# Optimization experiments

Hardware: AMD Instinct MI355X
Metric: run time of the kernel (lower is better)

## Reference

```python
import jax, jax.numpy as jnp
import numpy as np

B, T, D, H, DH, W = 2, 2048, 512, 8, 64, 64  # batch, seq, d_model, heads, d_head, window
BASE = 10000.0


def rope(x):
    # x: [b, t, d]; rotate-half RoPE applied over the full feature dim (as in source: pos_enc on d_model)
    d = x.shape[-1]
    half = d // 2
    inv_freq = BASE ** (-jnp.arange(half, dtype=jnp.float32) / half)          # [half]
    ang = jnp.arange(x.shape[1], dtype=jnp.float32)[:, None] * inv_freq       # [t, half]
    cos, sin = jnp.cos(ang), jnp.sin(ang)
    x1, x2 = x[..., :half], x[..., half:]
    return jnp.concatenate([x1 * cos - x2 * sin, x1 * sin + x2 * cos], axis=-1)


def setup_inputs() -> dict:
    key = jax.random.key(0)
    k0, k1, k2, k3 = jax.random.split(key, 4)
    x = jax.random.normal(k0, (B, T, D), jnp.float32)
    Wq = jax.random.normal(k1, (D, D), jnp.float32) / jnp.sqrt(D)
    Wkv = jax.random.normal(k2, (D, 2 * D), jnp.float32) / jnp.sqrt(D)
    # NOTE: source zero-inits lin; we use random weights so the output/grads are non-trivial
    Wlin = jax.random.normal(k3, (D, D), jnp.float32) / jnp.sqrt(D)
    blin = jnp.zeros((D,), jnp.float32)
    return {"x": x, "Wq": Wq, "Wkv": Wkv, "Wlin": Wlin, "blin": blin}


def reference(x, Wq, Wkv, Wlin, blin):
    b, t, _ = x.shape
    scale = DH ** -0.5
    q = rope(x @ Wq).reshape(b, t, H, DH).transpose(0, 2, 1, 3)               # [b,h,t,d]
    kv = x @ Wkv
    k, v = kv[..., :D], kv[..., D:]
    k = rope(k).reshape(b, t, H, DH).transpose(0, 2, 1, 3)                    # [b,h,t,d]
    v = v.reshape(b, t, H, DH).transpose(0, 2, 1, 3)                          # [b,h,t,d]
    pad = [(0, 0), (0, 0), (W - 1, 0), (0, 0)]
    kp, vp = jnp.pad(k, pad), jnp.pad(v, pad)                                 # [b,h,t+W-1,d]
    idx = jnp.arange(t)[:, None] + jnp.arange(W)[None, :]                     # [t,W] sliding-window gather
    kw, vw = kp[:, :, idx], vp[:, :, idx]                                     # [b,h,t,W,d]
    attn = jax.nn.softmax(jnp.einsum('bhtd,bhtwd->bhtw', q, kw) * scale, axis=-1)
    out = jnp.einsum('bhtw,bhtwd->bhtd', attn, vw)                            # [b,h,t,d]
    out = out.transpose(0, 2, 1, 3).reshape(b, t, D)
    return out @ Wlin + blin
```

## Files before the change

### kernel.cpp

```cpp
#include <hip/hip_runtime.h>
#include <cstddef>

#define T_N 2048
#define M_N 4096
#define KW  512

typedef __attribute__((ext_vector_type(4))) float f32x4;
typedef _Float16 f16x8 __attribute__((ext_vector_type(8)));
typedef _Float16 f16x2 __attribute__((ext_vector_type(2)));

#define GLOAD_LDS(g, l) __builtin_amdgcn_global_load_lds( \
    (const __attribute__((address_space(1))) unsigned int*)(g), \
    (__attribute__((address_space(3))) unsigned int*)(l), 16, 0, 0)

__global__ __launch_bounds__(256) void prep(
    const float* __restrict__ x, const float* __restrict__ Wq,
    const float* __restrict__ Wkv, const float* __restrict__ Wlin,
    _Float16* __restrict__ Axp, _Float16* __restrict__ Wcatp,
    _Float16* __restrict__ Wlinp, _Float16* __restrict__ tab16) {
  __shared__ float tile[64][65];
  const int bid = blockIdx.x;
  const int tid = threadIdx.x;
  if (bid < 1024) {
    int idx = bid * 256 + tid;
    int m = idx >> 6, k8 = (idx & 63) << 3;
    const float* src = x + (size_t)m * 512 + k8;
    const float4 a = *(const float4*)src;
    const float4 b = *(const float4*)(src + 4);
    f16x8 o;
    o[0] = (_Float16)a.x; o[1] = (_Float16)a.y; o[2] = (_Float16)a.z; o[3] = (_Float16)a.w;
    o[4] = (_Float16)b.x; o[5] = (_Float16)b.y; o[6] = (_Float16)b.z; o[7] = (_Float16)b.w;
    *(f16x8*)(Axp + (size_t)m * 512 + k8) = o;
    return;
  }
  if (bid >= 1280) {
    int gid = (bid - 1280) * 256 + tid;
    int t = gid >> 8, f = gid & 255;
    float invf = exp2f(-0.05190512648261503f * (float)f);
    float s, c;
    sincosf((float)t * invf, &s, &c);
    f16x2 cs;
    cs[0] = (_Float16)c; cs[1] = (_Float16)s;
    *(f16x2*)(tab16 + 2 * ((size_t)t * 256 + f)) = cs;
    return;
  }
  int wb = bid - 1024;
  const float* W; int N; int mode; int bx, by;
  if (wb < 64)       { W = Wq;   N = 512;  mode = 0; bx = wb & 7;  by = wb >> 3; }
  else if (wb < 192) { wb -= 64;  W = Wkv; N = 1024; mode = 1; bx = wb & 15; by = wb >> 4; }
  else               { wb -= 192; W = Wlin; N = 512; mode = 2; bx = wb & 7;  by = wb >> 3; }
  const int n0 = bx * 64, k0 = by * 64;
#pragma unroll
  for (int it = 0; it < 16; ++it) {
    int idx = tid + it * 256;
    int r = idx >> 6, c = idx & 63;
    tile[r][c] = W[(size_t)(k0 + r) * N + n0 + c];
  }
  __syncthreads();
#pragma unroll
  for (int it = 0; it < 16; ++it) {
    int idx = tid + it * 256;
    int n = idx >> 6, kk = idx & 63;
    int cg = n0 + n;
    int np; _Float16* out;
    if (mode == 0)      { np = 2 * (cg & 255) + (cg >> 8); out = Wcatp; }
    else if (mode == 1) { np = (cg < 512) ? 512 + 2 * (cg & 255) + (cg >> 8)
                                          : 1024 + (cg - 512);
                          out = Wcatp; }
    else                { np = cg; out = Wlinp; }
    out[(size_t)np * KW + k0 + kk] = (_Float16)tile[kk][n];
  }
}

__global__ __launch_bounds__(256) void gemm_qkv_rope(
    const _Float16* __restrict__ Ap, const _Float16* __restrict__ Bp,
    const _Float16* __restrict__ tab16, _Float16* __restrict__ Qh,
    _Float16* __restrict__ Kh, _Float16* __restrict__ Vh) {
  __shared__ __align__(16) _Float16 sm[64 * 64 + 128 * 64];
  _Float16* sA = sm;
  _Float16* sB = sm + 64 * 64;
  const int tid = threadIdx.x;
  const int wid = tid >> 6, lane = tid & 63;
  const int il = lane & 15, g = lane >> 4;
  const int m0 = blockIdx.y * 64, n0 = blockIdx.x * 128;
  const int wm = (wid >> 1) * 32, wn = (wid & 1) * 64;
  f32x4 acc[2][4] = {};

  const _Float16* ga = Ap + (size_t)(m0 + wid * 16 + (lane >> 3)) * KW + (lane & 7) * 8;
  const _Float16* gb = Bp + (size_t)(n0 + wid * 32 + (lane >> 3)) * KW + (lane & 7) * 8;
  _Float16* la = sA + wid * 16 * 64;
  _Float16* lb = sB + wid * 32 * 64;

  for (int k0 = 0; k0 < KW; k0 += 64) {
    GLOAD_LDS(ga + k0, la);
    GLOAD_LDS(ga + 8 * KW + k0, la + 8 * 64);
#pragma unroll
    for (int p = 0; p < 4; ++p)
      GLOAD_LDS(gb + (size_t)(p * 8) * KW + k0, lb + p * 8 * 64);
    __syncthreads();
#pragma unroll
    for (int ks = 0; ks < 2; ++ks) {
      f16x8 af[2], bf[4];
#pragma unroll
      for (int i = 0; i < 2; ++i)
        af[i] = *(const f16x8*)&sA[(wm + i * 16 + il) * 64 + ks * 32 + g * 8];
#pragma unroll
      for (int j = 0; j < 4; ++j)
        bf[j] = *(const f16x8*)&sB[(wn + j * 16 + il) * 64 + ks * 32 + g * 8];
#pragma unroll
      for (int i = 0; i < 2; ++i)
#pragma unroll
        for (int j = 0; j < 4; ++j)
          acc[i][j] = __builtin_amdgcn_mfma_f32_16x16x32_f16(af[i], bf[j], acc[i][j], 0, 0, 0);
    }
    __syncthreads();
  }
  const int b8 = (m0 >> 11) * 8;
  const int tb = m0 & (T_N - 1);
  const bool isv = (n0 >= 1024);
  const bool isk = (n0 >= 512) && !isv;
  _Float16* OT  = sm;
  _Float16* OTV = sm;

  if (isv) {
#pragma unroll
    for (int i = 0; i < 2; ++i)
#pragma unroll
      for (int j = 0; j < 4; ++j) {
        f32x4 v = acc[i][j];
        int col = wn + 16 * j + il;
#pragma unroll
        for (int r = 0; r < 4; ++r) {
          int tl = wm + i * 16 + g * 4 + r;
          OTV[col * 72 + tl] = (_Float16)v[r];
        }
      }
    __syncthreads();
    const int cv = n0 - 1024;
#pragma unroll
    for (int it = 0; it < 4; ++it) {
      int c = tid + it * 256;
      int col = c >> 3, t8 = (c & 7) * 8;
      int h = (cv + col) >> 6, d = (cv + col) & 63;
      *(f16x8*)(Vh + ((size_t)(b8 + h) * 64 + d) * T_N + tb + t8) =
          *(const f16x8*)&OTV[col * 72 + t8];
    }
    return;
  }
  const int n0p = n0 - (isk ? 512 : 0);
  const int h0 = n0p >> 7;
#pragma unroll
  for (int i = 0; i < 2; ++i) {
#pragma unroll
    for (int j = 0; j < 4; ++j) {
      f32x4 v = acc[i][j];
#pragma unroll
      for (int r = 0; r < 4; ++r) {
        float self = v[r];
        float part = __shfl_xor(self, 1);
        int tl = wm + i * 16 + g * 4 + r;
        int tpos = tb + tl;
        int p = il & 1;
        int f = (n0p + wn + 16 * j + (il & 14)) >> 1;
        f16x2 cs = *(const f16x2*)(tab16 + 2 * ((size_t)tpos * 256 + f));
        float c = (float)cs[0], s = (float)cs[1];
        float o = p ? (self * c + part * s) : (self * c - part * s);
        OT[(p * 64 + tl) * 72 + (f & 63)] = (_Float16)o;
      }
    }
  }
  __syncthreads();
  _Float16* dst = isk ? Kh : Qh;
#pragma unroll
  for (int it = 0; it < 4; ++it) {
    int c = tid + it * 256;
    int p = c >> 9, row = (c >> 3) & 63, d8 = (c & 7) * 8;
    *(f16x8*)(dst + ((size_t)(b8 + h0 + 4 * p) * T_N + tb + row) * 64 + d8) =
        *(const f16x8*)&OT[(p * 64 + row) * 72 + d8];
  }
}

#define RQ 72
#define RK 72
#define RV 104
#define RP 104
#define RO 72

__global__ __launch_bounds__(256, 4) void attn_fused(
    const _Float16* __restrict__ Qh, const _Float16* __restrict__ Kh,
    const _Float16* __restrict__ Vh, _Float16* __restrict__ Aout) {
  __shared__ __align__(16) _Float16 sm[19200];
  __shared__ float pm[2][32];
  __shared__ float ps[2][32];
  _Float16* Ks  = sm;
  _Float16* Qs  = sm + 6912;
  _Float16* VTs = sm + 9216;
  _Float16* Ps  = sm + 15872;
  _Float16* OH  = sm;

  const int wgid = blockIdx.x;
  const int orig = (wgid & 7) * 128 + (wgid >> 3);
  const int tile = orig & 63;
  const int h = (orig >> 6) & 7;
  const int b = orig >> 9;
  const int t0 = tile * 32;
  const int tid = threadIdx.x;
  const size_t bh = (size_t)(b * 8 + h);

  {
    int i = tid >> 3, d8 = (tid & 7) * 8;
    *(f16x8*)(Qs + i * RQ + d8) =
        *(const f16x8*)(Qh + (bh * T_N + t0 + i) * 64 + d8);
  }
#pragma unroll
  for (int itn = 0; itn < 3; ++itn) {
    int c = tid + itn * 256;
    int jr = c >> 3, d8 = (c & 7) * 8;
    int p = t0 - 64 + jr;
    f16x8 o = {};
    if (p >= 0) o = *(const f16x8*)(Kh + (bh * T_N + p) * 64 + d8);
    *(f16x8*)(Ks + jr * RK + d8) = o;
  }
#pragma unroll
  for (int itn = 0; itn < 3; ++itn) {
    int c = tid + itn * 256;
    int d = c & 63, jr8 = (c >> 6) * 8;
    int p8 = t0 - 64 + jr8;
    f16x8 o = {};
    if (p8 >= 0) o = *(const f16x8*)(Vh + (bh * 64 + d) * T_N + p8);
    *(f16x8*)(VTs + d * RV + jr8) = o;
  }
  __syncthreads();

  const int lane = tid & 63;
  const int il = lane & 15, g = lane >> 4;
  const int w = tid >> 6;
  const int it = w & 1, jh = w >> 1;
  const int i_q = 16 * it + il;

  f32x4 sacc[3] = {};
  {
    f16x8 qf0 = *(const f16x8*)(Qs + i_q * RQ + 8 * g);
    f16x8 qf1 = *(const f16x8*)(Qs + i_q * RQ + 32 + 8 * g);
#pragma unroll
    for (int jt = 0; jt < 3; ++jt) {
      int jrow = 16 * (3 * jh + jt) + il;
      f16x8 a0 = *(const f16x8*)(Ks + jrow * RK + 8 * g);
      f16x8 a1 = *(const f16x8*)(Ks + jrow * RK + 32 + 8 * g);
      sacc[jt] = __builtin_amdgcn_mfma_f32_16x16x32_f16(a0, qf0, sacc[jt], 0, 0, 0);
      sacc[jt] = __builtin_amdgcn_mfma_f32_16x16x32_f16(a1, qf1, sacc[jt], 0, 0, 0);
    }
  }
  float mx = -3e38f;
#pragma unroll
  for (int jt = 0; jt < 3; ++jt)
#pragma unroll
    for (int r = 0; r < 4; ++r) {
      int j = 16 * (3 * jh + jt) + 4 * g + r;
      int wv = j - 1 - i_q;
      if (wv >= 0 && wv < 64) mx = fmaxf(mx, sacc[jt][r]);
    }
  mx = fmaxf(mx, __shfl_xor(mx, 16));
  mx = fmaxf(mx, __shfl_xor(mx, 32));
  if (g == 0) pm[jh][i_q] = mx;
  __syncthreads();
  {
    const float m = fmaxf(pm[0][i_q], pm[1][i_q]);
    float sum = 0.f;
#pragma unroll
    for (int jt = 0; jt < 3; ++jt)
#pragma unroll
      for (int r = 0; r < 4; ++r) {
        int j = 16 * (3 * jh + jt) + 4 * g + r;
        int wv = j - 1 - i_q;
        float ex = 0.f;
        if (wv >= 0 && wv < 64) {
          ex = exp2f((sacc[jt][r] - m) * 0.18033688011112042f);
          sum += ex;
        }
        Ps[i_q * RP + j] = (_Float16)ex;
      }
    sum += __shfl_xor(sum, 16);
    sum += __shfl_xor(sum, 32);
    if (g == 0) ps[jh][i_q] = sum;
  }
  __syncthreads();

  f32x4 oacc[2] = {};
#pragma unroll
  for (int ks = 0; ks < 3; ++ks) {
    f16x8 pf = *(const f16x8*)(Ps + i_q * RP + 32 * ks + 8 * g);
#pragma unroll
    for (int q2 = 0; q2 < 2; ++q2) {
      int dt = jh + 2 * q2;
      f16x8 vf = *(const f16x8*)(VTs + (16 * dt + il) * RV + 32 * ks + 8 * g);
      oacc[q2] = __builtin_amdgcn_mfma_f32_16x16x32_f16(pf, vf, oacc[q2], 0, 0, 0);
    }
  }
#pragma unroll
  for (int r = 0; r < 4; ++r) {
    int i = 16 * it + 4 * g + r;
    float inv = 1.f / (ps[0][i] + ps[1][i]);
#pragma unroll
    for (int q2 = 0; q2 < 2; ++q2) {
      int d = 16 * (jh + 2 * q2) + il;
      OH[i * RO + d] = (_Float16)(oacc[q2][r] * inv);
    }
  }
  __syncthreads();
  {
    int i = tid >> 3, d8 = (tid & 7) * 8;
    *(f16x8*)(Aout + ((size_t)(b * T_N + t0 + i)) * 512 + h * 64 + d8) =
        *(const f16x8*)(OH + i * RO + d8);
  }
}

__global__ __launch_bounds__(256) void gemm_out(
    const _Float16* __restrict__ Ap, const _Float16* __restrict__ Bp,
    const float* __restrict__ bias, float* __restrict__ C) {
  __shared__ __align__(16) _Float16 sA[64 * 64];
  __shared__ __align__(16) _Float16 sB[64 * 64];
  const int tid = threadIdx.x;
  const int wid = tid >> 6, lane = tid & 63;
  const int il = lane & 15, g = lane >> 4;
  const int m0 = blockIdx.y * 64, n0 = blockIdx.x * 64;
  const int wm = (wid >> 1) * 32, wn = (wid & 1) * 32;
  f32x4 acc[2][2] = {};

  const _Float16* ga = Ap + (size_t)(m0 + wid * 16 + (lane >> 3)) * KW + (lane & 7) * 8;
  const _Float16* gb = Bp + (size_t)(n0 + wid * 16 + (lane >> 3)) * KW + (lane & 7) * 8;
  _Float16* la = sA + wid * 16 * 64;
  _Float16* lb = sB + wid * 16 * 64;

  for (int k0 = 0; k0 < KW; k0 += 64) {
    GLOAD_LDS(ga + k0, la);
    GLOAD_LDS(ga + 8 * KW + k0, la + 8 * 64);
    GLOAD_LDS(gb + k0, lb);
    GLOAD_LDS(gb + 8 * KW + k0, lb + 8 * 64);
    __syncthreads();
#pragma unroll
    for (int ks = 0; ks < 2; ++ks) {
      f16x8 af[2], bf[2];
#pragma unroll
      for (int i = 0; i < 2; ++i)
        af[i] = *(const f16x8*)&sA[(wm + i * 16 + il) * 64 + ks * 32 + g * 8];
#pragma unroll
      for (int j = 0; j < 2; ++j)
        bf[j] = *(const f16x8*)&sB[(wn + j * 16 + il) * 64 + ks * 32 + g * 8];
#pragma unroll
      for (int i = 0; i < 2; ++i)
#pragma unroll
        for (int j = 0; j < 2; ++j)
          acc[i][j] = __builtin_amdgcn_mfma_f32_16x16x32_f16(af[i], bf[j], acc[i][j], 0, 0, 0);
    }
    __syncthreads();
  }
  const int cn = n0 + wn + il;
  const int rbase = m0 + wm + g * 4;
#pragma unroll
  for (int j = 0; j < 2; ++j) {
    float badd = bias[cn + j * 16];
#pragma unroll
    for (int i = 0; i < 2; ++i)
#pragma unroll
      for (int r = 0; r < 4; ++r)
        C[(size_t)(rbase + i * 16 + r) * 512 + cn + j * 16] = acc[i][j][r] + badd;
  }
}

extern "C" void kernel_launch(void* const* d_in, const int* in_sizes, int n_in,
                              void* d_out, int out_size, void* d_ws, size_t ws_size,
                              hipStream_t stream) {
  const float* x    = (const float*)d_in[0];
  const float* Wq   = (const float*)d_in[1];
  const float* Wkv  = (const float*)d_in[2];
  const float* Wlin = (const float*)d_in[3];
  const float* blin = (const float*)d_in[4];
  float* out = (float*)d_out;

  char* ws = (char*)d_ws;
  _Float16* Axp   = (_Float16*)(ws);
  _Float16* Wcatp = (_Float16*)(ws + 4194304);
  _Float16* Wlinp = (_Float16*)(ws + 5767168);
  _Float16* tab16 = (_Float16*)(ws + 6291456);
  _Float16* Qh    = (_Float16*)(ws + 8388608);
  _Float16* Kh    = (_Float16*)(ws + 12582912);
  _Float16* Vh    = (_Float16*)(ws + 16777216);
  _Float16* Aaop  = (_Float16*)(ws + 20971520);

  prep<<<3328, 256, 0, stream>>>(x, Wq, Wkv, Wlin, Axp, Wcatp, Wlinp, tab16);
  gemm_qkv_rope<<<dim3(12, 64), 256, 0, stream>>>(Axp, Wcatp, tab16, Qh, Kh, Vh);
  attn_fused<<<1024, 256, 0, stream>>>(Qh, Kh, Vh, Aaop);
  gemm_out<<<dim3(8, 64), 256, 0, stream>>>(Aaop, Wlinp, blin, out);
}
```

Before: 104.1 us.

## Enlarge attention query tile to 64 rows and keep softmax per-wave

The sliding-window attention kernel now processes 64 queries per workgroup instead of 32, so each loaded K/V block (128 keys) is shared by more queries. This cuts redundant K/V loads. Each wave now owns 16 full query rows, so the max and sum reductions stay inside the wave and the cross-wave LDS exchange and two barriers go away. The cost is more LDS per block, launch bounds dropping from 4 to 2 blocks per CU, and half as many workgroups.

```diff
diff --git a/kernel.cpp b/kernel.cpp
--- a/kernel.cpp
+++ b/kernel.cpp
@@ -7,6 +7,7 @@
 
 typedef __attribute__((ext_vector_type(4))) float f32x4;
 typedef _Float16 f16x8 __attribute__((ext_vector_type(8)));
+typedef _Float16 f16x4 __attribute__((ext_vector_type(4)));
 typedef _Float16 f16x2 __attribute__((ext_vector_type(2)));
 
 #define GLOAD_LDS(g, l) __builtin_amdgcn_global_load_lds( \
@@ -180,138 +181,136 @@
   }
 }
 
-#define RQ 72
-#define RK 72
-#define RV 104
-#define RP 104
-#define RO 72
-
-__global__ __launch_bounds__(256, 4) void attn_fused(
+__global__ __launch_bounds__(256, 2) void attn_fused(
     const _Float16* __restrict__ Qh, const _Float16* __restrict__ Kh,
     const _Float16* __restrict__ Vh, _Float16* __restrict__ Aout) {
-  __shared__ __align__(16) _Float16 sm[19200];
-  __shared__ float pm[2][32];
-  __shared__ float ps[2][32];
+  __shared__ __align__(16) _Float16 sm[31232];
   _Float16* Ks  = sm;
-  _Float16* Qs  = sm + 6912;
   _Float16* VTs = sm + 9216;
-  _Float16* Ps  = sm + 15872;
+  _Float16* Qs  = sm + 17920;
+  _Float16* Ps  = sm + 22528;
   _Float16* OH  = sm;
 
   const int wgid = blockIdx.x;
-  const int orig = (wgid & 7) * 128 + (wgid >> 3);
-  const int tile = orig & 63;
-  const int h = (orig >> 6) & 7;
-  const int b = orig >> 9;
-  const int t0 = tile * 32;
+  const int orig = (wgid & 7) * 64 + (wgid >> 3);
+  const int tile = orig & 31;
+  const int h = (orig >> 5) & 7;
+  const int b = orig >> 8;
+  const int t0 = tile * 64;
   const int tid = threadIdx.x;
   const size_t bh = (size_t)(b * 8 + h);
 
-  {
-    int i = tid >> 3, d8 = (tid & 7) * 8;
-    *(f16x8*)(Qs + i * RQ + d8) =
-        *(const f16x8*)(Qh + (bh * T_N + t0 + i) * 64 + d8);
-  }
-#pragma unroll
-  for (int itn = 0; itn < 3; ++itn) {
+#pragma unroll
+  for (int itn = 0; itn < 2; ++itn) {
+    int c = tid + itn * 256;
+    int row = c >> 3, d8 = (c & 7) * 8;
+    *(f16x8*)(Qs + row * 72 + d8) =
+        *(const f16x8*)(Qh + (bh * T_N + t0 + row) * 64 + d8);
+  }
+#pragma unroll
+  for (int itn = 0; itn < 4; ++itn) {
     int c = tid + itn * 256;
     int jr = c >> 3, d8 = (c & 7) * 8;
     int p = t0 - 64 + jr;
     f16x8 o = {};
     if (p >= 0) o = *(const f16x8*)(Kh + (bh * T_N + p) * 64 + d8);
-    *(f16x8*)(Ks + jr * RK + d8) = o;
-  }
-#pragma unroll
-  for (int itn = 0; itn < 3; ++itn) {
+    *(f16x8*)(Ks + jr * 72 + d8) = o;
+  }
+#pragma unroll
+  for (int itn = 0; itn < 4; ++itn) {
     int c = tid + itn * 256;
     int d = c & 63, jr8 = (c >> 6) * 8;
     int p8 = t0 - 64 + jr8;
     f16x8 o = {};
     if (p8 >= 0) o = *(const f16x8*)(Vh + (bh * 64 + d) * T_N + p8);
-    *(f16x8*)(VTs + d * RV + jr8) = o;
+    *(f16x8*)(VTs + d * 136 + jr8) = o;
   }
   __syncthreads();
 
   const int lane = tid & 63;
   const int il = lane & 15, g = lane >> 4;
-  const int w = tid >> 6;
-  const int it = w & 1, jh = w >> 1;
+  const int it = tid >> 6;
   const int i_q = 16 * it + il;
 
-  f32x4 sacc[3] = {};
+  f32x4 sacc[5] = {};
   {
-    f16x8 qf0 = *(const f16x8*)(Qs + i_q * RQ + 8 * g);
-    f16x8 qf1 = *(const f16x8*)(Qs + i_q * RQ + 32 + 8 * g);
-#pragma unroll
-    for (int jt = 0; jt < 3; ++jt) {
-      int jrow = 16 * (3 * jh + jt) + il;
-      f16x8 a0 = *(const f16x8*)(Ks + jrow * RK + 8 * g);
-      f16x8 a1 = *(const f16x8*)(Ks + jrow * RK + 32 + 8 * g);
-      sacc[jt] = __builtin_amdgcn_mfma_f32_16x16x32_f16(a0, qf0, sacc[jt], 0, 0, 0);
-      sacc[jt] = __builtin_amdgcn_mfma_f32_16x16x32_f16(a1, qf1, sacc[jt], 0, 0, 0);
+    f16x8 qf0 = *(const f16x8*)(Qs + i_q * 72 + 8 * g);
+    f16x8 qf1 = *(const f16x8*)(Qs + i_q * 72 + 32 + 8 * g);
+#pragma unroll
+    for (int jt5 = 0; jt5 < 5; ++jt5) {
+      int jrow = 16 * (it + jt5) + il;
+      f16x8 a0 = *(const f16x8*)(Ks + jrow * 72 + 8 * g);
+      f16x8 a1 = *(const f16x8*)(Ks + jrow * 72 + 32 + 8 * g);
+      sacc[jt5] = __builtin_amdgcn_mfma_f32_16x16x32_f16(a0, qf0, sacc[jt5], 0, 0, 0);
+      sacc[jt5] = __builtin_amdgcn_mfma_f32_16x16x32_f16(a1, qf1, sacc[jt5], 0, 0, 0);
     }
   }
   float mx = -3e38f;
 #pragma unroll
-  for (int jt = 0; jt < 3; ++jt)
+  for (int jt5 = 0; jt5 < 5; ++jt5)
 #pragma unroll
     for (int r = 0; r < 4; ++r) {
-      int j = 16 * (3 * jh + jt) + 4 * g + r;
+      int j = 16 * (it + jt5) + 4 * g + r;
       int wv = j - 1 - i_q;
-      if (wv >= 0 && wv < 64) mx = fmaxf(mx, sacc[jt][r]);
+      if (wv >= 0 && wv < 64) mx = fmaxf(mx, sacc[jt5][r]);
     }
   mx = fmaxf(mx, __shfl_xor(mx, 16));
   mx = fmaxf(mx, __shfl_xor(mx, 32));
-  if (g == 0) pm[jh][i_q] = mx;
-  __syncthreads();
+  float sum = 0.f;
+#pragma unroll
+  for (int jt5 = 0; jt5 < 5; ++jt5) {
+    f16x4 pv;
+#pragma unroll
+    for (int r = 0; r < 4; ++r) {
+      int j = 16 * (it + jt5) + 4 * g + r;
+      int wv = j - 1 - i_q;
+      float ex = 0.f;
+      if (wv >= 0 && wv < 64) {
+        ex = exp2f((sacc[jt5][r] - mx) * 0.18033688011112042f);
+        sum += ex;
+      }
+      pv[r] = (_Float16)ex;
+    }
+    *(f16x4*)(Ps + i_q * 136 + 16 * (it + jt5) + 4 * g) = pv;
+  }
+  sum += __shfl_xor(sum, 16);
+  sum += __shfl_xor(sum, 32);
   {
-    const float m = fmaxf(pm[0][i_q], pm[1][i_q]);
-    float sum = 0.f;
-#pragma unroll
-    for (int jt = 0; jt < 3; ++jt)
-#pragma unroll
-      for (int r = 0; r < 4; ++r) {
-        int j = 16 * (3 * jh + jt) + 4 * g + r;
-        int wv = j - 1 - i_q;
-        float ex = 0.f;
-        if (wv >= 0 && wv < 64) {
-          ex = exp2f((sacc[jt][r] - m) * 0.18033688011112042f);
-          sum += ex;
-        }
-        Ps[i_q * RP + j] = (_Float16)ex;
-      }
-    sum += __shfl_xor(sum, 16);
-    sum += __shfl_xor(sum, 32);
-    if (g == 0) ps[jh][i_q] = sum;
-  }
-  __syncthreads();
-
-  f32x4 oacc[2] = {};
+    int jtz = (it & 1) ? (it - 1) : (it + 5);
+    f16x4 z = {};
+    *(f16x4*)(Ps + i_q * 136 + 16 * jtz + 4 * g) = z;
+  }
+
+  const int jb = 32 * (it >> 1);
+  f32x4 oacc[4] = {};
 #pragma unroll
   for (int ks = 0; ks < 3; ++ks) {
-    f16x8 pf = *(const f16x8*)(Ps + i_q * RP + 32 * ks + 8 * g);
-#pragma unroll
-    for (int q2 = 0; q2 < 2; ++q2) {
-      int dt = jh + 2 * q2;
-      f16x8 vf = *(const f16x8*)(VTs + (16 * dt + il) * RV + 32 * ks + 8 * g);
-      oacc[q2] = __builtin_amdgcn_mfma_f32_16x16x32_f16(pf, vf, oacc[q2], 0, 0, 0);
-    }
-  }
+    f16x8 pf = *(const f16x8*)(Ps + i_q * 136 + jb + 32 * ks + 8 * g);
+#pragma unroll
+    for (int dt = 0; dt < 4; ++dt) {
+      f16x8 vf = *(const f16x8*)(VTs + (16 * dt + il) * 136 + jb + 32 * ks + 8 * g);
+      oacc[dt] = __builtin_amdgcn_mfma_f32_16x16x32_f16(pf, vf, oacc[dt], 0, 0, 0);
+    }
+  }
+  __syncthreads();
 #pragma unroll
   for (int r = 0; r < 4; ++r) {
+    float s4 = __shfl(sum, 4 * g + r);
+    float inv = 1.f / s4;
     int i = 16 * it + 4 * g + r;
-    float inv = 1.f / (ps[0][i] + ps[1][i]);
-#pragma unroll
-    for (int q2 = 0; q2 < 2; ++q2) {
-      int d = 16 * (jh + 2 * q2) + il;
-      OH[i * RO + d] = (_Float16)(oacc[q2][r] * inv);
-    }
-  }
-  __syncthreads();
-  {
-    int i = tid >> 3, d8 = (tid & 7) * 8;
-    *(f16x8*)(Aout + ((size_t)(b * T_N + t0 + i)) * 512 + h * 64 + d8) =
-        *(const f16x8*)(OH + i * RO + d8);
+#pragma unroll
+    for (int dt = 0; dt < 4; ++dt) {
+      int d = 16 * dt + il;
+      OH[i * 72 + d] = (_Float16)(oacc[dt][r] * inv);
+    }
+  }
+  __syncthreads();
+#pragma unroll
+  for (int itn = 0; itn < 2; ++itn) {
+    int c = tid + itn * 256;
+    int row = c >> 3, d8 = (c & 7) * 8;
+    *(f16x8*)(Aout + ((size_t)(b * T_N + t0 + row)) * 512 + h * 64 + d8) =
+        *(const f16x8*)(OH + row * 72 + d8);
   }
 }
 
@@ -390,6 +389,6 @@
 
   prep<<<3328, 256, 0, stream>>>(x, Wq, Wkv, Wlin, Axp, Wcatp, Wlinp, tab16);
   gemm_qkv_rope<<<dim3(12, 64), 256, 0, stream>>>(Axp, Wcatp, tab16, Qh, Kh, Vh);
-  attn_fused<<<1024, 256, 0, stream>>>(Qh, Kh, Vh, Aaop);
+  attn_fused<<<512, 256, 0, stream>>>(Qh, Kh, Vh, Aaop);
   gemm_out<<<dim3(8, 64), 256, 0, stream>>>(Aaop, Wlinp, blin, out);
 }
```

Result: no change. 104.1 us (+0.1%).
